# Optimization experiments

Hardware: AMD Instinct MI355X
Metric: run time of the kernel (lower is better)

The kernel has to match this reference:

```python
import jax, jax.numpy as jnp
import numpy as np

B = 16384
NEG = 10
V = 100000
E = 128

def setup_inputs() -> dict:
    key = jax.random.key(0)
    k1, k2, k3, k4, k5 = jax.random.split(key, 5)
    input_word = jax.random.randint(k1, (B,), 0, V)
    context_word = jax.random.randint(k2, (B,), 0, V)
    noise_words = jax.random.randint(k3, (B * NEG,), 0, V)
    # torch init: uniform_(-1, 1)
    W_in = jax.random.uniform(k4, (V, E), jnp.float32, -1.0, 1.0)
    W_ctx = jax.random.uniform(k5, (V, E), jnp.float32, -1.0, 1.0)
    return {"input_word": input_word, "context_word": context_word,
            "noise_words": noise_words, "W_in": W_in, "W_ctx": W_ctx}

def reference(input_word, context_word, noise_words, W_in, W_ctx):
    center = W_in[input_word]               # [B, E]
    ctx = W_ctx[context_word]               # [B, E]
    # positive score: per-example dot product
    out_loss = jax.nn.log_sigmoid(jnp.einsum('be,be->b', ctx, center))  # [B]
    noise = W_ctx[noise_words].reshape(B, NEG, E)                       # [B, NEG, E]
    # negative scores: -u_k . v_c
    neg_scores = -jnp.einsum('bke,be->bk', noise, center)               # [B, NEG]
    noise_loss = jax.nn.log_sigmoid(neg_scores).sum(axis=1)             # [B]
    return -(out_loss + noise_loss).mean()
```

## Files before the change

### kernel.cpp

```cpp
#include <hip/hip_runtime.h>
#include <hip/hip_bf16.h>

constexpr int kB   = 16384;
constexpr int kNeg = 10;
constexpr int kE   = 128;
constexpr int kWavesPerBlock = 4;
constexpr int kExPerWave     = 2;
constexpr int kBlocks = kB / (kWavesPerBlock * kExPerWave);

__device__ __forceinline__ float log_sigmoid(float x) {
    return fminf(x, 0.0f) - log1pf(expf(-fabsf(x)));
}

__device__ __forceinline__ float dot4(float4 a, float4 b) {
    return a.x * b.x + a.y * b.y + a.z * b.z + a.w * b.w;
}

__global__ __launch_bounds__(256, 4) void w2v_loss_kernel(
    const int*   __restrict__ input_word,
    const int*   __restrict__ context_word,
    const int*   __restrict__ noise_words,
    const float* __restrict__ W_in,
    const float* __restrict__ W_ctx,
    float*       __restrict__ partials)
{
    const int lane = threadIdx.x & 63;
    const int wave = threadIdx.x >> 6;
    const int half = lane >> 5;
    const int l32  = lane & 31;

    const int b = (blockIdx.x * kWavesPerBlock + wave) * kExPerWave + half;

    const int iw = input_word[b];
    const int cw = context_word[b];
    int nw[kNeg];
    #pragma unroll
    for (int k = 0; k < kNeg; ++k)
        nw[k] = noise_words[b * kNeg + k];

    const float4 c = ((const float4*)(W_in  + (size_t)iw * kE))[l32];
    const float4 x = ((const float4*)(W_ctx + (size_t)cw * kE))[l32];
    float4 nv[kNeg];
    #pragma unroll
    for (int k = 0; k < kNeg; ++k)
        nv[k] = ((const float4*)(W_ctx + (size_t)nw[k] * kE))[l32];

    float pos = dot4(c, x);
    float negp[kNeg];
    #pragma unroll
    for (int k = 0; k < kNeg; ++k)
        negp[k] = dot4(c, nv[k]);

    #pragma unroll
    for (int off = 16; off > 0; off >>= 1) {
        pos += __shfl_xor(pos, off);
        #pragma unroll
        for (int k = 0; k < kNeg; ++k)
            negp[k] += __shfl_xor(negp[k], off);
    }

    float v = pos;
    #pragma unroll
    for (int k = 0; k < kNeg; ++k)
        v = (l32 == k + 1) ? -negp[k] : v;
    float s = (l32 < 1 + kNeg) ? log_sigmoid(v) : 0.0f;

    #pragma unroll
    for (int off = 16; off > 0; off >>= 1)
        s += __shfl_xor(s, off);
    s += __shfl_xor(s, 32);

    __shared__ float smem[kWavesPerBlock];
    if (lane == 0) smem[wave] = s;
    __syncthreads();
    if (threadIdx.x == 0)
        partials[blockIdx.x] = smem[0] + smem[1] + smem[2] + smem[3];
}

__global__ __launch_bounds__(256) void w2v_reduce_kernel(
    const float* __restrict__ partials,
    float*       __restrict__ out)
{
    float acc = 0.0f;
    for (int i = threadIdx.x; i < kBlocks; i += 256)
        acc += partials[i];

    #pragma unroll
    for (int off = 32; off > 0; off >>= 1)
        acc += __shfl_xor(acc, off);

    __shared__ float smem[4];
    const int lane = threadIdx.x & 63;
    const int wave = threadIdx.x >> 6;
    if (lane == 0) smem[wave] = acc;
    __syncthreads();
    if (threadIdx.x == 0) {
        const float total = smem[0] + smem[1] + smem[2] + smem[3];
        out[0] = -total / (float)kB;
    }
}

extern "C" void kernel_launch(void* const* d_in, const int* in_sizes, int n_in,
                              void* d_out, int out_size, void* d_ws, size_t ws_size,
                              hipStream_t stream) {
    const int*   input_word   = (const int*)d_in[0];
    const int*   context_word = (const int*)d_in[1];
    const int*   noise_words  = (const int*)d_in[2];
    const float* W_in         = (const float*)d_in[3];
    const float* W_ctx        = (const float*)d_in[4];
    float*       out          = (float*)d_out;
    float*       partials     = (float*)d_ws;

    w2v_loss_kernel<<<kBlocks, 256, 0, stream>>>(
        input_word, context_word, noise_words, W_in, W_ctx, partials);
    w2v_reduce_kernel<<<1, 256, 0, stream>>>(partials, out);
}
```

Measured before the change: 126.3 us.

## Map one example per wave, splitting its context rows across wave halves

Each wave now handles a single example instead of two. The 11 W_ctx rows (context plus 10 noise) are split between the two 32-lane halves, 6 and 5 rows, with both halves loading the same center row. This halves per-thread register demand (6 float4 instead of 11) and the shuffle-reduction work, and raises the occupancy hint to 8. In exchange it launches twice as many blocks and loads the center vector redundantly in each half, which may add L2 traffic.

New measurement: 126.9 us. About the same (+0.5%).

```diff
diff --git a/kernel.cpp b/kernel.cpp
--- a/kernel.cpp
+++ b/kernel.cpp
@@ -1,12 +1,10 @@
 #include <hip/hip_runtime.h>
-#include <hip/hip_bf16.h>
 
 constexpr int kB   = 16384;
 constexpr int kNeg = 10;
 constexpr int kE   = 128;
 constexpr int kWavesPerBlock = 4;
-constexpr int kExPerWave     = 2;
-constexpr int kBlocks = kB / (kWavesPerBlock * kExPerWave);
+constexpr int kBlocks = kB / kWavesPerBlock;
 
 __device__ __forceinline__ float log_sigmoid(float x) {
     return fminf(x, 0.0f) - log1pf(expf(-fabsf(x)));
@@ -16,7 +14,7 @@
     return a.x * b.x + a.y * b.y + a.z * b.z + a.w * b.w;
 }
 
-__global__ __launch_bounds__(256, 4) void w2v_loss_kernel(
+__global__ __launch_bounds__(256, 8) void w2v_loss_kernel(
     const int*   __restrict__ input_word,
     const int*   __restrict__ context_word,
     const int*   __restrict__ noise_words,
@@ -24,12 +22,13 @@
     const float* __restrict__ W_ctx,
     float*       __restrict__ partials)
 {
-    const int lane = threadIdx.x & 63;
-    const int wave = threadIdx.x >> 6;
+    const int tid  = threadIdx.x;
+    const int wave = tid >> 6;
+    const int lane = tid & 63;
     const int half = lane >> 5;
     const int l32  = lane & 31;
 
-    const int b = (blockIdx.x * kWavesPerBlock + wave) * kExPerWave + half;
+    const int b = __builtin_amdgcn_readfirstlane(blockIdx.x * kWavesPerBlock + wave);
 
     const int iw = input_word[b];
     const int cw = context_word[b];
@@ -38,32 +37,39 @@
     for (int k = 0; k < kNeg; ++k)
         nw[k] = noise_words[b * kNeg + k];
 
-    const float4 c = ((const float4*)(W_in  + (size_t)iw * kE))[l32];
-    const float4 x = ((const float4*)(W_ctx + (size_t)cw * kE))[l32];
-    float4 nv[kNeg];
+    int ridx[6];
+    ridx[0] = half ? nw[5] : cw;
     #pragma unroll
-    for (int k = 0; k < kNeg; ++k)
-        nv[k] = ((const float4*)(W_ctx + (size_t)nw[k] * kE))[l32];
+    for (int j = 1; j <= 4; ++j)
+        ridx[j] = half ? nw[5 + j] : nw[j - 1];
+    ridx[5] = half ? cw : nw[4];
 
-    float pos = dot4(c, x);
-    float negp[kNeg];
+    const float4 c = ((const float4*)(W_in + (size_t)iw * kE))[l32];
+    float4 r[6];
     #pragma unroll
-    for (int k = 0; k < kNeg; ++k)
-        negp[k] = dot4(c, nv[k]);
+    for (int j = 0; j < 6; ++j)
+        r[j] = ((const float4*)(W_ctx + (size_t)ridx[j] * kE))[l32];
+
+    float d[6];
+    #pragma unroll
+    for (int j = 0; j < 6; ++j)
+        d[j] = dot4(c, r[j]);
 
     #pragma unroll
     for (int off = 16; off > 0; off >>= 1) {
-        pos += __shfl_xor(pos, off);
         #pragma unroll
-        for (int k = 0; k < kNeg; ++k)
-            negp[k] += __shfl_xor(negp[k], off);
+        for (int j = 0; j < 6; ++j)
+            d[j] += __shfl_xor(d[j], off);
     }
 
-    float v = pos;
+    float v = d[0];
     #pragma unroll
-    for (int k = 0; k < kNeg; ++k)
-        v = (l32 == k + 1) ? -negp[k] : v;
-    float s = (l32 < 1 + kNeg) ? log_sigmoid(v) : 0.0f;
+    for (int j = 1; j < 6; ++j)
+        v = (l32 == j) ? d[j] : v;
+    const bool isPos = (half == 0) && (l32 == 0);
+    v = isPos ? v : -v;
+    const bool active = half ? (l32 < 5) : (l32 < 6);
+    float s = active ? log_sigmoid(v) : 0.0f;
 
     #pragma unroll
     for (int off = 16; off > 0; off >>= 1)
@@ -73,7 +79,7 @@
     __shared__ float smem[kWavesPerBlock];
     if (lane == 0) smem[wave] = s;
     __syncthreads();
-    if (threadIdx.x == 0)
+    if (tid == 0)
         partials[blockIdx.x] = smem[0] + smem[1] + smem[2] + smem[3];
 }
 
```

## Fuse loss and reduction into one cooperative kernel with grid sync

Applied to the files above, without the earlier changes.

Replaces the two-kernel scheme (per-block partials, then a single-block reduce) with one cooperative launch of 1024 blocks. Each block handles two passes of examples, then a grid-wide sync lets block 0 sum the partials and write the final loss. The aim is to drop the second kernel launch and its gap. In exchange it adds grid-sync overhead and a cap on resident blocks, and it keeps a fallback to the old two-kernel path if the cooperative launch fails.

Result: slower. 244.7 us (+93.8%).

```diff
diff --git a/kernel.cpp b/kernel.cpp
--- a/kernel.cpp
+++ b/kernel.cpp
@@ -1,12 +1,14 @@
 #include <hip/hip_runtime.h>
-#include <hip/hip_bf16.h>
+#include <hip/hip_cooperative_groups.h>
+
+namespace cg = cooperative_groups;
 
 constexpr int kB   = 16384;
 constexpr int kNeg = 10;
 constexpr int kE   = 128;
-constexpr int kWavesPerBlock = 4;
-constexpr int kExPerWave     = 2;
-constexpr int kBlocks = kB / (kWavesPerBlock * kExPerWave);
+
+constexpr int kCoopBlocks = 1024;
+constexpr int kPasses     = kB / (kCoopBlocks * 8);
 
 __device__ __forceinline__ float log_sigmoid(float x) {
     return fminf(x, 0.0f) - log1pf(expf(-fabsf(x)));
@@ -16,21 +18,14 @@
     return a.x * b.x + a.y * b.y + a.z * b.z + a.w * b.w;
 }
 
-__global__ __launch_bounds__(256, 4) void w2v_loss_kernel(
+__device__ __forceinline__ float wave_pass(
+    int b, int l32, int half,
     const int*   __restrict__ input_word,
     const int*   __restrict__ context_word,
     const int*   __restrict__ noise_words,
     const float* __restrict__ W_in,
-    const float* __restrict__ W_ctx,
-    float*       __restrict__ partials)
+    const float* __restrict__ W_ctx)
 {
-    const int lane = threadIdx.x & 63;
-    const int wave = threadIdx.x >> 6;
-    const int half = lane >> 5;
-    const int l32  = lane & 31;
-
-    const int b = (blockIdx.x * kWavesPerBlock + wave) * kExPerWave + half;
-
     const int iw = input_word[b];
     const int cw = context_word[b];
     int nw[kNeg];
@@ -69,11 +64,79 @@
     for (int off = 16; off > 0; off >>= 1)
         s += __shfl_xor(s, off);
     s += __shfl_xor(s, 32);
+    return s;
+}
 
-    __shared__ float smem[kWavesPerBlock];
+__global__ __launch_bounds__(256, 4) void w2v_fused(
+    const int*   __restrict__ input_word,
+    const int*   __restrict__ context_word,
+    const int*   __restrict__ noise_words,
+    const float* __restrict__ W_in,
+    const float* __restrict__ W_ctx,
+    float*       __restrict__ partials,
+    float*       __restrict__ out)
+{
+    const int tid  = threadIdx.x;
+    const int wave = tid >> 6;
+    const int lane = tid & 63;
+    const int half = lane >> 5;
+    const int l32  = lane & 31;
+
+    float wsum = 0.0f;
+    #pragma unroll
+    for (int pass = 0; pass < kPasses; ++pass) {
+        const int b = ((pass * kCoopBlocks + blockIdx.x) * 4 + wave) * 2 + half;
+        wsum += wave_pass(b, l32, half,
+                          input_word, context_word, noise_words, W_in, W_ctx);
+    }
+
+    __shared__ float smem[4];
+    if (lane == 0) smem[wave] = wsum;
+    __syncthreads();
+    if (tid == 0)
+        partials[blockIdx.x] = smem[0] + smem[1] + smem[2] + smem[3];
+
+    cg::this_grid().sync();
+
+    if (blockIdx.x == 0) {
+        float acc = 0.0f;
+        for (int i = tid; i < kCoopBlocks; i += 256)
+            acc += partials[i];
+        #pragma unroll
+        for (int off = 32; off > 0; off >>= 1)
+            acc += __shfl_xor(acc, off);
+        __shared__ float sm2[4];
+        if (lane == 0) sm2[wave] = acc;
+        __syncthreads();
+        if (tid == 0)
+            out[0] = -(sm2[0] + sm2[1] + sm2[2] + sm2[3]) / (float)kB;
+    }
+}
+
+constexpr int kFbBlocks = kB / 8;
+
+__global__ __launch_bounds__(256, 4) void w2v_loss_kernel(
+    const int*   __restrict__ input_word,
+    const int*   __restrict__ context_word,
+    const int*   __restrict__ noise_words,
+    const float* __restrict__ W_in,
+    const float* __restrict__ W_ctx,
+    float*       __restrict__ partials)
+{
+    const int tid  = threadIdx.x;
+    const int wave = tid >> 6;
+    const int lane = tid & 63;
+    const int half = lane >> 5;
+    const int l32  = lane & 31;
+    const int b = (blockIdx.x * 4 + wave) * 2 + half;
+
+    const float s = wave_pass(b, l32, half,
+                              input_word, context_word, noise_words, W_in, W_ctx);
+
+    __shared__ float smem[4];
     if (lane == 0) smem[wave] = s;
     __syncthreads();
-    if (threadIdx.x == 0)
+    if (tid == 0)
         partials[blockIdx.x] = smem[0] + smem[1] + smem[2] + smem[3];
 }
 
@@ -82,22 +145,18 @@
     float*       __restrict__ out)
 {
     float acc = 0.0f;
-    for (int i = threadIdx.x; i < kBlocks; i += 256)
+    for (int i = threadIdx.x; i < kFbBlocks; i += 256)
         acc += partials[i];
-
     #pragma unroll
     for (int off = 32; off > 0; off >>= 1)
         acc += __shfl_xor(acc, off);
-
     __shared__ float smem[4];
     const int lane = threadIdx.x & 63;
     const int wave = threadIdx.x >> 6;
     if (lane == 0) smem[wave] = acc;
     __syncthreads();
-    if (threadIdx.x == 0) {
-        const float total = smem[0] + smem[1] + smem[2] + smem[3];
-        out[0] = -total / (float)kB;
-    }
+    if (threadIdx.x == 0)
+        out[0] = -(smem[0] + smem[1] + smem[2] + smem[3]) / (float)kB;
 }
 
 extern "C" void kernel_launch(void* const* d_in, const int* in_sizes, int n_in,
@@ -111,7 +170,16 @@
     float*       out          = (float*)d_out;
     float*       partials     = (float*)d_ws;
 
-    w2v_loss_kernel<<<kBlocks, 256, 0, stream>>>(
-        input_word, context_word, noise_words, W_in, W_ctx, partials);
-    w2v_reduce_kernel<<<1, 256, 0, stream>>>(partials, out);
+    void* args[] = {
+        (void*)&input_word, (void*)&context_word, (void*)&noise_words,
+        (void*)&W_in, (void*)&W_ctx, (void*)&partials, (void*)&out
+    };
+    hipError_t err = hipLaunchCooperativeKernel(
+        (const void*)w2v_fused, dim3(kCoopBlocks), dim3(256), args, 0, stream);
+
+    if (err != hipSuccess) {
+        w2v_loss_kernel<<<kFbBlocks, 256, 0, stream>>>(
+            input_word, context_word, noise_words, W_in, W_ctx, partials);
+        w2v_reduce_kernel<<<1, 256, 0, stream>>>(partials, out);
+    }
 }
```
